# Kernel optimization log

Hardware: AMD Instinct MI355X
Metric: run time of the kernel (lower is better)

The kernel has to match this reference:

```python
import jax, jax.numpy as jnp
import numpy as np

BLOCK_SIZE = 16
NVFP4_LEVELS = np.array([0.0, 0.5, 1.0, 1.5, 2.0, 3.0, 4.0, 6.0], dtype=np.float32)


def quantize_to_nvfp4(x, block_size=BLOCK_SIZE):
    """NVFP4 fake-quant: per-16-element block, scale = amax/6, round |x| to nearest level."""
    levels = jnp.asarray(NVFP4_LEVELS, dtype=x.dtype)
    orig_shape = x.shape
    xf = x.reshape(-1, block_size)                                   # [nblk, 16]
    amax = jnp.clip(jnp.max(jnp.abs(xf), axis=-1, keepdims=True), 1e-12)
    scale = amax / 6.0                                               # [nblk, 1]
    x_norm = jnp.abs(xf) / scale                                     # in [0, 6]
    idx = jnp.argmin(jnp.abs(x_norm[..., None] - levels), axis=-1)   # nearest level (first on ties, like torch)
    x_q = jnp.sign(xf) * levels[idx] * scale
    return x_q.reshape(orig_shape)


def _magnitude_mask_2_4(w):
    # keep 2 largest-|.| of every group of 4 along in_features (row-wise 2:4)
    out_f, in_f = w.shape
    a = jnp.abs(w).reshape(out_f, in_f // 4, 4)
    thr = jnp.sort(a, axis=-1)[..., 2:3]          # 2nd-largest magnitude in group
    mask = (a >= thr).reshape(out_f, in_f)
    return mask.astype(w.dtype)


def setup_inputs() -> dict:
    key = jax.random.key(0)
    k_x, k_w, k_s, k_a, k_b, k_bias = jax.random.split(key, 6)
    B, S, IN_F, OUT_F, RANK = 2, 2048, 4096, 4096, 32
    x = jax.random.normal(k_x, (B, S, IN_F), dtype=jnp.float32)
    smooth_scale = jax.random.uniform(k_s, (IN_F,), dtype=jnp.float32, minval=0.5, maxval=2.0)
    # realistic calibrated weight: 2:4 magnitude-sparse then NVFP4 fake-quantized
    w = jax.random.normal(k_w, (OUT_F, IN_F), dtype=jnp.float32) * 0.02
    w_sparse = w * _magnitude_mask_2_4(w)
    w_quantized = quantize_to_nvfp4(w_sparse)
    lora_a = jax.random.normal(k_a, (RANK, IN_F), dtype=jnp.float32) * 0.02
    lora_b = jax.random.normal(k_b, (OUT_F, RANK), dtype=jnp.float32) * 0.02
    bias = jax.random.normal(k_bias, (OUT_F,), dtype=jnp.float32)
    return {"x": x, "smooth_scale": smooth_scale, "w_quantized": w_quantized,
            "lora_a": lora_a, "lora_b": lora_b, "bias": bias}


def reference(x, smooth_scale, w_quantized, lora_a, lora_b, bias):
    # x: [B, S, IN], smooth_scale: [IN], w_quantized: [OUT, IN]
    x_smoothed = x * smooth_scale                                    # SmoothQuant activation scaling
    x_q = quantize_to_nvfp4(x_smoothed, BLOCK_SIZE)                  # block fake-quant of activations
    base_out = jnp.einsum('bsi,oi->bso', x_q, w_quantized)           # 2:4-sparse quantized matmul
    svd_out = jnp.einsum('bsr,or->bso',
                         jnp.einsum('bsi,ri->bsr', x_smoothed, lora_a), lora_b)  # low-rank correction
    return base_out + svd_out + bias
```

## Files before the change

### kernel.cpp

```cpp
#include <hip/hip_runtime.h>
#include <hip/hip_bf16.h>
#include <stdint.h>

typedef __attribute__((ext_vector_type(8)))  __bf16 bf16x8;
typedef __attribute__((ext_vector_type(4)))  float  f32x4;

#define KP 4224

__device__ inline void async_copy16(const void* g, void* l) {
  __builtin_amdgcn_global_load_lds((const __attribute__((address_space(1))) void*)g,
                                   (__attribute__((address_space(3))) void*)l, 16, 0, 0);
}

__global__ __launch_bounds__(256) void fused_quant_lora_kernel(
    const float* __restrict__ x, const float* __restrict__ ss,
    const float* __restrict__ la, __bf16* __restrict__ Ab,
    float* __restrict__ Tp) {
  __shared__ float red[4][16][32];
  int tid  = threadIdx.x;
  int m0   = blockIdx.x << 4;
  int by   = blockIdx.y;

  {
    int row = m0 + (tid >> 4);
    int cb0 = tid & 15;
#pragma unroll
    for (int i = 0; i < 2; i++) {
      int col = (by << 9) + ((cb0 + (i << 4)) << 4);
      const float4* xp = (const float4*)(x + ((size_t)row << 12) + col);
      const float4* sp = (const float4*)(ss + col);
      float xs[16];
#pragma unroll
      for (int j = 0; j < 4; j++) {
        float4 xv = xp[j]; float4 sv = sp[j];
        xs[4*j+0] = xv.x * sv.x; xs[4*j+1] = xv.y * sv.y;
        xs[4*j+2] = xv.z * sv.z; xs[4*j+3] = xv.w * sv.w;
      }
      float amax = 0.f;
#pragma unroll
      for (int j = 0; j < 16; j++) amax = fmaxf(amax, fabsf(xs[j]));
      amax = fmaxf(amax, 1e-12f);
      float scale = amax / 6.0f;
      bf16x8 o0, o1;
#pragma unroll
      for (int j = 0; j < 16; j++) {
        float a  = fabsf(xs[j]);
        float xn = a / scale;
        float lvl;
        if (xn < 2.25f) {
          lvl = 0.5f * __builtin_ceilf(__builtin_fmaf(2.0f, xn, -0.5f));
        } else {
          lvl = (xn <= 2.5f) ? 2.0f : (xn <= 3.5f) ? 3.0f
              : (xn <= 5.0f) ? 4.0f : 6.0f;
        }
        float mag = lvl * scale;
        float q = (xs[j] > 0.f) ? mag : ((xs[j] < 0.f) ? -mag : 0.f);
        if (j < 8) o0[j] = (__bf16)q; else o1[j-8] = (__bf16)q;
      }
      __bf16* dst = Ab + (size_t)row * KP + col;
      *(bf16x8*)dst = o0;
      *(bf16x8*)(dst + 8) = o1;
    }
  }

  {
    int wave = tid >> 6, lane = tid & 63;
    int lrow = lane & 15, kg = lane >> 4;
    int kbase = (by << 9) + (wave << 7);
    f32x4 acc0 = {0.f,0.f,0.f,0.f}, acc1 = {0.f,0.f,0.f,0.f};
    const float* xrow = x + ((size_t)(m0 + lrow) << 12);
    const float* a0   = la + ((size_t)lrow << 12);
    const float* a1   = a0 + (16 << 12);
#pragma unroll
    for (int k0 = 0; k0 < 128; k0 += 32) {
      int kk = kbase + k0 + (kg << 3);
      float xv[8], sv[8], v0[8], v1[8];
      *(float4*)&xv[0] = *(const float4*)(xrow + kk);
      *(float4*)&xv[4] = *(const float4*)(xrow + kk + 4);
      *(float4*)&sv[0] = *(const float4*)(ss + kk);
      *(float4*)&sv[4] = *(const float4*)(ss + kk + 4);
      *(float4*)&v0[0] = *(const float4*)(a0 + kk);
      *(float4*)&v0[4] = *(const float4*)(a0 + kk + 4);
      *(float4*)&v1[0] = *(const float4*)(a1 + kk);
      *(float4*)&v1[4] = *(const float4*)(a1 + kk + 4);
      bf16x8 af, b0, b1;
#pragma unroll
      for (int j = 0; j < 8; j++) {
        af[j] = (__bf16)(xv[j] * sv[j]);
        b0[j] = (__bf16)v0[j];
        b1[j] = (__bf16)v1[j];
      }
      acc0 = __builtin_amdgcn_mfma_f32_16x16x32_bf16(af, b0, acc0, 0, 0, 0);
      acc1 = __builtin_amdgcn_mfma_f32_16x16x32_bf16(af, b1, acc1, 0, 0, 0);
    }
#pragma unroll
    for (int r = 0; r < 4; r++) {
      red[wave][kg*4 + r][lrow]      = acc0[r];
      red[wave][kg*4 + r][16 + lrow] = acc1[r];
    }
    __syncthreads();
    for (int o = tid; o < 512; o += 256) {
      int rr = o >> 5, cc = o & 31;
      float s = red[0][rr][cc] + red[1][rr][cc] + red[2][rr][cc] + red[3][rr][cc];
      Tp[((size_t)by * 4096 + m0 + rr) * 32 + cc] = s;
    }
  }
}

__global__ __launch_bounds__(256) void wconv_fix_kernel(const float* __restrict__ w,
                                                        const float* __restrict__ lb,
                                                        const float* __restrict__ Tp,
                                                        __bf16* __restrict__ Bb,
                                                        __bf16* __restrict__ Ab) {
  int b = blockIdx.x;
  if (b < 8448) {
    int id  = b * 256 + threadIdx.x;
    int row = id / 528;
    int g   = id - row * 528;
    bf16x8 v;
    if (g < 512) {
      const float4* wp = (const float4*)(w + ((size_t)row << 12) + (g << 3));
      float4 a = wp[0], bb = wp[1];
      v[0]=(__bf16)a.x;  v[1]=(__bf16)a.y;  v[2]=(__bf16)a.z;  v[3]=(__bf16)a.w;
      v[4]=(__bf16)bb.x; v[5]=(__bf16)bb.y; v[6]=(__bf16)bb.z; v[7]=(__bf16)bb.w;
    } else if (g < 516) {
      const float* p = lb + (size_t)row * 32 + ((g - 512) << 3);
#pragma unroll
      for (int j = 0; j < 8; j++) v[j] = (__bf16)p[j];
    } else {
#pragma unroll
      for (int j = 0; j < 8; j++) v[j] = (__bf16)0.f;
    }
    *(bf16x8*)(Bb + (size_t)row * KP + ((size_t)g << 3)) = v;
  } else {
    int id  = (b - 8448) * 256 + threadIdx.x;
    int row = id >> 5, cc = id & 31;
    float s = 0.f;
#pragma unroll
    for (int kc = 0; kc < 8; kc++)
      s += Tp[((size_t)kc * 4096 + row) * 32 + cc];
    __bf16* dst = Ab + (size_t)row * KP + 4096;
    dst[cc]      = (__bf16)s;
    dst[32 + cc] = (__bf16)0.f;
    dst[64 + cc] = (__bf16)0.f;
    dst[96 + cc] = (__bf16)0.f;
  }
}

#define GBAR() __builtin_amdgcn_s_barrier()
#define PRI1() __builtin_amdgcn_s_setprio(1)
#define PRI0() __builtin_amdgcn_s_setprio(0)
#define WVM(n) asm volatile("s_waitcnt vmcnt(" #n ")" ::: "memory")

#define STG(srcb, dstb, bb, h, t) do {                                         \
    const __bf16* _s = (srcb) + (size_t)(h) * (128 * (size_t)KP)               \
                              + ((size_t)(t) << 6);                            \
    char* _d = (dstb) + ((bb) << 15) + ((h) << 14);                            \
    async_copy16(_s, _d);                                                      \
    async_copy16(_s + 32, _d + 1024);                                          \
  } while (0)

#define LD8(dst, p, off) do { _Pragma("unroll")                                \
  for (int u = 0; u < 8; u++)                                                  \
    dst[u] = *(const bf16x8*)((p) + (((off) + u) << 10)); } while (0)

#define LD4(dst, p, off) do { _Pragma("unroll")                                \
  for (int u = 0; u < 4; u++)                                                  \
    dst[u] = *(const bf16x8*)((p) + (((off) + u) << 10)); } while (0)

#define MMQ(Ar, Br, MFB, NFB) do {                                             \
  _Pragma("unroll") for (int mf = 0; mf < 4; mf++)                             \
  _Pragma("unroll") for (int nf = 0; nf < 2; nf++)                             \
  _Pragma("unroll") for (int ks = 0; ks < 2; ks++)                             \
    acc[(MFB)+mf][(NFB)+nf] = __builtin_amdgcn_mfma_f32_16x16x32_bf16(         \
        Ar[mf*2+ks], Br[nf*2+ks], acc[(MFB)+mf][(NFB)+nf], 0, 0, 0);           \
  } while (0)

__global__ __launch_bounds__(512, 2) void gemm_kernel(const __bf16* __restrict__ A,
                                                      const __bf16* __restrict__ B,
                                                      const float* __restrict__ bias,
                                                      float* __restrict__ C) {
  extern __shared__ char lds[];
  const int tid  = threadIdx.x;
  const int w    = tid >> 6, lane = tid & 63;
  const int ln15 = lane & 15, kg = lane >> 4;
  const int wm   = w >> 2, wn = w & 3;
  const int bid  = blockIdx.x;
  const int sbid = ((bid & 7) << 5) | (bid >> 3);
  const int bm   = sbid >> 4, bn = sbid & 15;
  const size_t m0 = (size_t)bm << 8, n0 = (size_t)bn << 8;

  const int rr = (w << 4) + (lane >> 2);
  const int kk = ((lane & 3) ^ (((lane >> 5) & 1) << 1)) << 3;
  const __bf16* aS = A + (m0 + rr) * (size_t)KP + kk;
  const __bf16* bS = B + (n0 + rr) * (size_t)KP + kk;
  char* dA = lds + (w << 11);
  char* dB = lds + 65536 + (w << 11);

  int inner = (ln15 << 6) + (kg << 4);
  inner ^= (ln15 & 8) << 2;
  const char* pA0 = lds + (wm << 14) + inner;
  const char* pA1 = pA0 + 32768;
  const char* pB0 = lds + 65536 + (wn << 13) + inner;
  const char* pB1 = pB0 + 32768;

  bf16x8 Ax[8], Ay[8], Bg0[4], Bg1[4];
  f32x4 acc[8][4];
#pragma unroll
  for (int i = 0; i < 8; i++)
#pragma unroll
    for (int j = 0; j < 4; j++) acc[i][j] = (f32x4){0.f, 0.f, 0.f, 0.f};

  STG(bS, dB, 0, 0, 0); STG(bS, dB, 0, 1, 0);
  STG(aS, dA, 0, 0, 0); STG(aS, dA, 0, 1, 0);
  STG(bS, dB, 1, 0, 1); STG(bS, dB, 1, 1, 1);
  WVM(4);
  GBAR();
  LD8(Ax, pA0, 0); LD4(Bg0, pB0, 0);

#pragma unroll 1
  for (int i = 0; i < 32; i++) {
    const int t1 = 2*i + 1, t2 = 2*i + 2, t3 = 2*i + 3;
    GBAR();
    STG(aS, dA, 1, 0, t1);
    LD8(Ay, pA0, 8); LD4(Bg1, pB0, 4);
    PRI1(); MMQ(Ax, Bg0, 0, 0); PRI0();
    GBAR();
    STG(aS, dA, 1, 1, t1);
    PRI1(); MMQ(Ax, Bg1, 0, 2); PRI0();
    GBAR();
    STG(bS, dB, 0, 0, t2);
    PRI1(); MMQ(Ay, Bg0, 4, 0); PRI0();
    WVM(2);
    GBAR();
    STG(bS, dB, 0, 1, t2);
    LD8(Ax, pA1, 0); LD4(Bg0, pB1, 0);
    PRI1(); MMQ(Ay, Bg1, 4, 2); PRI0();
    GBAR();
    STG(aS, dA, 0, 0, t2);
    LD8(Ay, pA1, 8); LD4(Bg1, pB1, 4);
    PRI1(); MMQ(Ax, Bg0, 0, 0); PRI0();
    GBAR();
    STG(aS, dA, 0, 1, t2);
    PRI1(); MMQ(Ax, Bg1, 0, 2); PRI0();
    GBAR();
    STG(bS, dB, 1, 0, t3);
    PRI1(); MMQ(Ay, Bg0, 4, 0); PRI0();
    WVM(2);
    GBAR();
    STG(bS, dB, 1, 1, t3);
    LD8(Ax, pA0, 0); LD4(Bg0, pB0, 0);
    PRI1(); MMQ(Ay, Bg1, 4, 2); PRI0();
  }

  GBAR();
  STG(aS, dA, 1, 0, 65);
  LD8(Ay, pA0, 8); LD4(Bg1, pB0, 4);
  PRI1(); MMQ(Ax, Bg0, 0, 0); PRI0();
  GBAR();
  STG(aS, dA, 1, 1, 65);
  PRI1(); MMQ(Ax, Bg1, 0, 2); PRI0();
  GBAR();
  PRI1(); MMQ(Ay, Bg0, 4, 0); PRI0();
  WVM(0);
  GBAR();
  LD8(Ax, pA1, 0); LD4(Bg0, pB1, 0);
  PRI1(); MMQ(Ay, Bg1, 4, 2); PRI0();
  GBAR();
  LD8(Ay, pA1, 8); LD4(Bg1, pB1, 4);
  PRI1(); MMQ(Ax, Bg0, 0, 0); PRI0();
  GBAR();
  PRI1(); MMQ(Ax, Bg1, 0, 2); PRI0();
  GBAR();
  PRI1(); MMQ(Ay, Bg0, 4, 0); PRI0();
  GBAR();
  PRI1(); MMQ(Ay, Bg1, 4, 2); PRI0();

  const int    colb = (int)n0 + (wn << 6) + ln15;
  const size_t rowb = m0 + ((size_t)wm << 7) + (kg << 2);
#pragma unroll
  for (int nf = 0; nf < 4; nf++) {
    const int col = colb + (nf << 4);
    const float bv = bias[col];
#pragma unroll
    for (int mf = 0; mf < 8; mf++) {
      const size_t r0 = rowb + ((size_t)mf << 4);
#pragma unroll
      for (int q = 0; q < 4; q++)
        C[(r0 + q) * 4096 + col] = acc[mf][nf][q] + bv;
    }
  }
}

extern "C" void kernel_launch(void* const* d_in, const int* in_sizes, int n_in,
                              void* d_out, int out_size, void* d_ws, size_t ws_size,
                              hipStream_t stream) {
  const float* x    = (const float*)d_in[0];
  const float* ss   = (const float*)d_in[1];
  const float* w    = (const float*)d_in[2];
  const float* la   = (const float*)d_in[3];
  const float* lb   = (const float*)d_in[4];
  const float* bias = (const float*)d_in[5];
  float* out = (float*)d_out;

  __bf16* Ab = (__bf16*)d_ws;
  __bf16* Bb = Ab + (size_t)4096 * KP;
  float* Tp = out;

  static bool s_attr = false;
  if (!s_attr) {
    hipFuncSetAttribute((const void*)gemm_kernel,
                        hipFuncAttributeMaxDynamicSharedMemorySize, 131072);
    s_attr = true;
  }

  fused_quant_lora_kernel<<<dim3(256, 8), 256, 0, stream>>>(x, ss, la, Ab, Tp);
  wconv_fix_kernel<<<8960, 256, 0, stream>>>(w, lb, Tp, Bb, Ab);
  gemm_kernel<<<256, 512, 131072, stream>>>(Ab, Bb, bias, out);
}
```

Measured before the change: 310.1 us.

## Merge prep kernels, shrink K padding, switch GEMM to 32x32x16 MFMA

```diff
diff --git a/kernel.cpp b/kernel.cpp
--- a/kernel.cpp
+++ b/kernel.cpp
@@ -4,24 +4,27 @@
 
 typedef __attribute__((ext_vector_type(8)))  __bf16 bf16x8;
 typedef __attribute__((ext_vector_type(4)))  float  f32x4;
-
-#define KP 4224
+typedef __attribute__((ext_vector_type(16))) float  f32x16;
+
+#define KP 4160
 
 __device__ inline void async_copy16(const void* g, void* l) {
   __builtin_amdgcn_global_load_lds((const __attribute__((address_space(1))) void*)g,
                                    (__attribute__((address_space(3))) void*)l, 16, 0, 0);
 }
 
-__global__ __launch_bounds__(256) void fused_quant_lora_kernel(
+__global__ __launch_bounds__(256) void prep_kernel(
     const float* __restrict__ x, const float* __restrict__ ss,
-    const float* __restrict__ la, __bf16* __restrict__ Ab,
-    float* __restrict__ Tp) {
+    const float* __restrict__ w, const float* __restrict__ la,
+    const float* __restrict__ lb, __bf16* __restrict__ Ab,
+    __bf16* __restrict__ Bb) {
   __shared__ float red[4][16][32];
-  int tid  = threadIdx.x;
-  int m0   = blockIdx.x << 4;
-  int by   = blockIdx.y;
-
-  {
+  int b   = blockIdx.x;
+  int tid = threadIdx.x;
+
+  if (b < 2048) {
+    int m0 = (b >> 3) << 4;
+    int by = b & 7;
     int row = m0 + (tid >> 4);
     int cb0 = tid & 15;
 #pragma unroll
@@ -61,19 +64,36 @@
       *(bf16x8*)dst = o0;
       *(bf16x8*)(dst + 8) = o1;
     }
-  }
-
-  {
+  } else if (b < 10368) {
+    int id  = (b - 2048) * 256 + tid;
+    int row = id / 520;
+    int g   = id - row * 520;
+    bf16x8 v;
+    if (g < 512) {
+      const float4* wp = (const float4*)(w + ((size_t)row << 12) + (g << 3));
+      float4 a = wp[0], bb = wp[1];
+      v[0]=(__bf16)a.x;  v[1]=(__bf16)a.y;  v[2]=(__bf16)a.z;  v[3]=(__bf16)a.w;
+      v[4]=(__bf16)bb.x; v[5]=(__bf16)bb.y; v[6]=(__bf16)bb.z; v[7]=(__bf16)bb.w;
+    } else if (g < 516) {
+      const float* p = lb + (size_t)row * 32 + ((g - 512) << 3);
+#pragma unroll
+      for (int j = 0; j < 8; j++) v[j] = (__bf16)p[j];
+    } else {
+#pragma unroll
+      for (int j = 0; j < 8; j++) v[j] = (__bf16)0.f;
+    }
+    *(bf16x8*)(Bb + (size_t)row * KP + ((size_t)g << 3)) = v;
+  } else {
+    int j16  = (b - 10368) << 4;
     int wave = tid >> 6, lane = tid & 63;
     int lrow = lane & 15, kg = lane >> 4;
-    int kbase = (by << 9) + (wave << 7);
     f32x4 acc0 = {0.f,0.f,0.f,0.f}, acc1 = {0.f,0.f,0.f,0.f};
-    const float* xrow = x + ((size_t)(m0 + lrow) << 12);
+    const float* xrow = x + ((size_t)(j16 + lrow) << 12);
     const float* a0   = la + ((size_t)lrow << 12);
     const float* a1   = a0 + (16 << 12);
-#pragma unroll
-    for (int k0 = 0; k0 < 128; k0 += 32) {
-      int kk = kbase + k0 + (kg << 3);
+#pragma unroll 4
+    for (int k0 = 0; k0 < 32; k0++) {
+      int kk = (wave << 10) + (k0 << 5) + (kg << 3);
       float xv[8], sv[8], v0[8], v1[8];
       *(float4*)&xv[0] = *(const float4*)(xrow + kk);
       *(float4*)&xv[4] = *(const float4*)(xrow + kk + 4);
@@ -85,10 +105,10 @@
       *(float4*)&v1[4] = *(const float4*)(a1 + kk + 4);
       bf16x8 af, b0, b1;
 #pragma unroll
-      for (int j = 0; j < 8; j++) {
-        af[j] = (__bf16)(xv[j] * sv[j]);
-        b0[j] = (__bf16)v0[j];
-        b1[j] = (__bf16)v1[j];
+      for (int q = 0; q < 8; q++) {
+        af[q] = (__bf16)(xv[q] * sv[q]);
+        b0[q] = (__bf16)v0[q];
+        b1[q] = (__bf16)v1[q];
       }
       acc0 = __builtin_amdgcn_mfma_f32_16x16x32_bf16(af, b0, acc0, 0, 0, 0);
       acc1 = __builtin_amdgcn_mfma_f32_16x16x32_bf16(af, b1, acc1, 0, 0, 0);
@@ -102,48 +122,10 @@
     for (int o = tid; o < 512; o += 256) {
       int rr = o >> 5, cc = o & 31;
       float s = red[0][rr][cc] + red[1][rr][cc] + red[2][rr][cc] + red[3][rr][cc];
-      Tp[((size_t)by * 4096 + m0 + rr) * 32 + cc] = s;
-    }
-  }
-}
-
-__global__ __launch_bounds__(256) void wconv_fix_kernel(const float* __restrict__ w,
-                                                        const float* __restrict__ lb,
-                                                        const float* __restrict__ Tp,
-                                                        __bf16* __restrict__ Bb,
-                                                        __bf16* __restrict__ Ab) {
-  int b = blockIdx.x;
-  if (b < 8448) {
-    int id  = b * 256 + threadIdx.x;
-    int row = id / 528;
-    int g   = id - row * 528;
-    bf16x8 v;
-    if (g < 512) {
-      const float4* wp = (const float4*)(w + ((size_t)row << 12) + (g << 3));
-      float4 a = wp[0], bb = wp[1];
-      v[0]=(__bf16)a.x;  v[1]=(__bf16)a.y;  v[2]=(__bf16)a.z;  v[3]=(__bf16)a.w;
-      v[4]=(__bf16)bb.x; v[5]=(__bf16)bb.y; v[6]=(__bf16)bb.z; v[7]=(__bf16)bb.w;
-    } else if (g < 516) {
-      const float* p = lb + (size_t)row * 32 + ((g - 512) << 3);
-#pragma unroll
-      for (int j = 0; j < 8; j++) v[j] = (__bf16)p[j];
-    } else {
-#pragma unroll
-      for (int j = 0; j < 8; j++) v[j] = (__bf16)0.f;
-    }
-    *(bf16x8*)(Bb + (size_t)row * KP + ((size_t)g << 3)) = v;
-  } else {
-    int id  = (b - 8448) * 256 + threadIdx.x;
-    int row = id >> 5, cc = id & 31;
-    float s = 0.f;
-#pragma unroll
-    for (int kc = 0; kc < 8; kc++)
-      s += Tp[((size_t)kc * 4096 + row) * 32 + cc];
-    __bf16* dst = Ab + (size_t)row * KP + 4096;
-    dst[cc]      = (__bf16)s;
-    dst[32 + cc] = (__bf16)0.f;
-    dst[64 + cc] = (__bf16)0.f;
-    dst[96 + cc] = (__bf16)0.f;
+      __bf16* dst = Ab + (size_t)(j16 + rr) * KP + 4096;
+      dst[cc]      = (__bf16)s;
+      dst[32 + cc] = (__bf16)0.f;
+    }
   }
 }
 
@@ -160,21 +142,21 @@
     async_copy16(_s + 32, _d + 1024);                                          \
   } while (0)
 
-#define LD8(dst, p, off) do { _Pragma("unroll")                                \
-  for (int u = 0; u < 8; u++)                                                  \
-    dst[u] = *(const bf16x8*)((p) + (((off) + u) << 10)); } while (0)
-
-#define LD4(dst, p, off) do { _Pragma("unroll")                                \
-  for (int u = 0; u < 4; u++)                                                  \
-    dst[u] = *(const bf16x8*)((p) + (((off) + u) << 10)); } while (0)
-
-#define MMQ(Ar, Br, MFB, NFB) do {                                             \
-  _Pragma("unroll") for (int mf = 0; mf < 4; mf++)                             \
-  _Pragma("unroll") for (int nf = 0; nf < 2; nf++)                             \
-  _Pragma("unroll") for (int ks = 0; ks < 2; ks++)                             \
-    acc[(MFB)+mf][(NFB)+nf] = __builtin_amdgcn_mfma_f32_16x16x32_bf16(         \
-        Ar[mf*2+ks], Br[nf*2+ks], acc[(MFB)+mf][(NFB)+nf], 0, 0, 0);           \
-  } while (0)
+#define KOFF(KS) ((((KS) >> 1) << 10) + ((((KS) & 1) << 5) ^ sx))
+
+#define RD_A(base, KS) do { _Pragma("unroll")                                  \
+  for (int mf = 0; mf < 4; mf++)                                               \
+    af[mf] = *(const bf16x8*)((base) + (mf << 12) + KOFF(KS)); } while (0)
+
+#define RD_B(base, KS) do {                                                    \
+    Br[0*4 + (KS)] = *(const bf16x8*)((base) + KOFF(KS));                      \
+    Br[1*4 + (KS)] = *(const bf16x8*)((base) + 4096 + KOFF(KS)); } while (0)
+
+#define MM8(KS) do { _Pragma("unroll")                                         \
+  for (int mf = 0; mf < 4; mf++) _Pragma("unroll")                             \
+  for (int nf = 0; nf < 2; nf++)                                               \
+    acc[mf][nf] = __builtin_amdgcn_mfma_f32_32x32x16_bf16(                     \
+        af[mf], Br[nf*4 + (KS)], acc[mf][nf], 0, 0, 0); } while (0)
 
 __global__ __launch_bounds__(512, 2) void gemm_kernel(const __bf16* __restrict__ A,
                                                       const __bf16* __restrict__ B,
@@ -183,7 +165,7 @@
   extern __shared__ char lds[];
   const int tid  = threadIdx.x;
   const int w    = tid >> 6, lane = tid & 63;
-  const int ln15 = lane & 15, kg = lane >> 4;
+  const int ln31 = lane & 31, kg2 = lane >> 5;
   const int wm   = w >> 2, wn = w & 3;
   const int bid  = blockIdx.x;
   const int sbid = ((bid & 7) << 5) | (bid >> 3);
@@ -197,97 +179,90 @@
   char* dA = lds + (w << 11);
   char* dB = lds + 65536 + (w << 11);
 
-  int inner = (ln15 << 6) + (kg << 4);
-  inner ^= (ln15 & 8) << 2;
-  const char* pA0 = lds + (wm << 14) + inner;
+  const int sx = (lane & 8) << 2;
+  const int cA = ((ln31 >> 4) << 11) + ((ln31 & 15) << 6) + (kg2 << 4);
+  const int cB = ((((wn & 1) << 2) + (ln31 >> 4)) << 11)
+               + ((ln31 & 15) << 6) + (kg2 << 4);
+  const char* pA0 = lds + (wm << 14) + cA;
   const char* pA1 = pA0 + 32768;
-  const char* pB0 = lds + 65536 + (wn << 13) + inner;
+  const char* pB0 = lds + 65536 + ((wn >> 1) << 14) + cB;
   const char* pB1 = pB0 + 32768;
 
-  bf16x8 Ax[8], Ay[8], Bg0[4], Bg1[4];
-  f32x4 acc[8][4];
-#pragma unroll
-  for (int i = 0; i < 8; i++)
-#pragma unroll
-    for (int j = 0; j < 4; j++) acc[i][j] = (f32x4){0.f, 0.f, 0.f, 0.f};
+  bf16x8 af[4], Br[8];
+  f32x16 acc[4][2];
+#pragma unroll
+  for (int i = 0; i < 4; i++)
+#pragma unroll
+    for (int j = 0; j < 2; j++)
+#pragma unroll
+      for (int q = 0; q < 16; q++) acc[i][j][q] = 0.f;
 
   STG(bS, dB, 0, 0, 0); STG(bS, dB, 0, 1, 0);
   STG(aS, dA, 0, 0, 0); STG(aS, dA, 0, 1, 0);
   STG(bS, dB, 1, 0, 1); STG(bS, dB, 1, 1, 1);
   WVM(4);
   GBAR();
-  LD8(Ax, pA0, 0); LD4(Bg0, pB0, 0);
 
 #pragma unroll 1
   for (int i = 0; i < 32; i++) {
-    const int t1 = 2*i + 1, t2 = 2*i + 2, t3 = 2*i + 3;
-    GBAR();
+    const int t1 = 2*i + 1, t2 = 2*i + 2;
+    int t3 = 2*i + 3; if (t3 > 64) t3 = 64;
     STG(aS, dA, 1, 0, t1);
-    LD8(Ay, pA0, 8); LD4(Bg1, pB0, 4);
-    PRI1(); MMQ(Ax, Bg0, 0, 0); PRI0();
+    RD_B(pB0, 0); RD_B(pB0, 1); RD_A(pA0, 0);
+    PRI1(); MM8(0); PRI0();
     GBAR();
     STG(aS, dA, 1, 1, t1);
-    PRI1(); MMQ(Ax, Bg1, 0, 2); PRI0();
+    RD_B(pB0, 2); RD_B(pB0, 3); RD_A(pA0, 1);
+    PRI1(); MM8(1); PRI0();
     GBAR();
     STG(bS, dB, 0, 0, t2);
-    PRI1(); MMQ(Ay, Bg0, 4, 0); PRI0();
-    WVM(2);
+    RD_A(pA0, 2);
+    PRI1(); MM8(2); PRI0();
     GBAR();
     STG(bS, dB, 0, 1, t2);
-    LD8(Ax, pA1, 0); LD4(Bg0, pB1, 0);
-    PRI1(); MMQ(Ay, Bg1, 4, 2); PRI0();
+    RD_A(pA0, 3);
+    PRI1(); MM8(3); PRI0();
+    WVM(4);
     GBAR();
     STG(aS, dA, 0, 0, t2);
-    LD8(Ay, pA1, 8); LD4(Bg1, pB1, 4);
-    PRI1(); MMQ(Ax, Bg0, 0, 0); PRI0();
+    RD_B(pB1, 0); RD_B(pB1, 1); RD_A(pA1, 0);
+    PRI1(); MM8(0); PRI0();
     GBAR();
     STG(aS, dA, 0, 1, t2);
-    PRI1(); MMQ(Ax, Bg1, 0, 2); PRI0();
+    RD_B(pB1, 2); RD_B(pB1, 3); RD_A(pA1, 1);
+    PRI1(); MM8(1); PRI0();
     GBAR();
     STG(bS, dB, 1, 0, t3);
-    PRI1(); MMQ(Ay, Bg0, 4, 0); PRI0();
-    WVM(2);
+    RD_A(pA1, 2);
+    PRI1(); MM8(2); PRI0();
     GBAR();
     STG(bS, dB, 1, 1, t3);
-    LD8(Ax, pA0, 0); LD4(Bg0, pB0, 0);
-    PRI1(); MMQ(Ay, Bg1, 4, 2); PRI0();
-  }
-
-  GBAR();
-  STG(aS, dA, 1, 0, 65);
-  LD8(Ay, pA0, 8); LD4(Bg1, pB0, 4);
-  PRI1(); MMQ(Ax, Bg0, 0, 0); PRI0();
-  GBAR();
-  STG(aS, dA, 1, 1, 65);
-  PRI1(); MMQ(Ax, Bg1, 0, 2); PRI0();
-  GBAR();
-  PRI1(); MMQ(Ay, Bg0, 4, 0); PRI0();
-  WVM(0);
-  GBAR();
-  LD8(Ax, pA1, 0); LD4(Bg0, pB1, 0);
-  PRI1(); MMQ(Ay, Bg1, 4, 2); PRI0();
-  GBAR();
-  LD8(Ay, pA1, 8); LD4(Bg1, pB1, 4);
-  PRI1(); MMQ(Ax, Bg0, 0, 0); PRI0();
-  GBAR();
-  PRI1(); MMQ(Ax, Bg1, 0, 2); PRI0();
-  GBAR();
-  PRI1(); MMQ(Ay, Bg0, 4, 0); PRI0();
-  GBAR();
-  PRI1(); MMQ(Ay, Bg1, 4, 2); PRI0();
-
-  const int    colb = (int)n0 + (wn << 6) + ln15;
-  const size_t rowb = m0 + ((size_t)wm << 7) + (kg << 2);
-#pragma unroll
-  for (int nf = 0; nf < 4; nf++) {
-    const int col = colb + (nf << 4);
+    RD_A(pA1, 3);
+    PRI1(); MM8(3); PRI0();
+    WVM(4);
+    GBAR();
+  }
+
+  RD_B(pB0, 0); RD_B(pB0, 1); RD_B(pB0, 2); RD_B(pB0, 3);
+  RD_A(pA0, 0); PRI1(); MM8(0); PRI0();
+  RD_A(pA0, 1); PRI1(); MM8(1); PRI0();
+  RD_A(pA0, 2); PRI1(); MM8(2); PRI0();
+  RD_A(pA0, 3); PRI1(); MM8(3); PRI0();
+
+  const int    colb = (int)n0 + (wn << 6) + ln31;
+  const size_t rowb = m0 + ((size_t)wm << 7) + (kg2 << 2);
+#pragma unroll
+  for (int nf = 0; nf < 2; nf++) {
+    const int col = colb + (nf << 5);
     const float bv = bias[col];
 #pragma unroll
-    for (int mf = 0; mf < 8; mf++) {
-      const size_t r0 = rowb + ((size_t)mf << 4);
-#pragma unroll
-      for (int q = 0; q < 4; q++)
-        C[(r0 + q) * 4096 + col] = acc[mf][nf][q] + bv;
+    for (int mf = 0; mf < 4; mf++) {
+      const size_t r0 = rowb + ((size_t)mf << 5);
+#pragma unroll
+      for (int q = 0; q < 16; q++) {
+        const size_t row = r0 + (q & 3) + ((q >> 2) << 3);
+        C[row * 4096 + col] = acc[mf][nf][q] + bv;
+      }
     }
   }
 }
@@ -305,7 +280,6 @@
 
   __bf16* Ab = (__bf16*)d_ws;
   __bf16* Bb = Ab + (size_t)4096 * KP;
-  float* Tp = out;
 
   static bool s_attr = false;
   if (!s_attr) {
@@ -314,7 +288,6 @@
     s_attr = true;
   }
 
-  fused_quant_lora_kernel<<<dim3(256, 8), 256, 0, stream>>>(x, ss, la, Ab, Tp);
-  wconv_fix_kernel<<<8960, 256, 0, stream>>>(w, lb, Tp, Bb, Ab);
+  prep_kernel<<<10624, 256, 0, stream>>>(x, ss, w, la, lb, Ab, Bb);
   gemm_kernel<<<256, 512, 131072, stream>>>(Ab, Bb, bias, out);
 }
```

Result: slower. 369.1 us (+19.0%).
